# Performance work log

Measured on AMD Instinct MI355X. Metric: run time of the kernel, lower is better.

## Reference

```python
import jax, jax.numpy as jnp
import numpy as np

N_NODES = 100000
N_EDGES = 1600000
IN_F = 128
HID = 128
OUT = 2


def setup_inputs() -> dict:
    key = jax.random.key(0)
    ks = jax.random.split(key, 12)
    s = lambda k, sh, f: jax.random.normal(k, sh, dtype=jnp.float32) * (1.0 / np.sqrt(f))
    return {
        "x": jax.random.normal(ks[0], (N_NODES, IN_F), dtype=jnp.float32),
        "W_self1": s(ks[1], (IN_F, HID), IN_F),
        "W_neigh1": s(ks[2], (IN_F, HID), IN_F),
        "b1": jnp.zeros((HID,), dtype=jnp.float32),
        "W_self2": s(ks[3], (HID, HID), HID),
        "W_neigh2": s(ks[4], (HID, HID), HID),
        "b2": jnp.zeros((HID,), dtype=jnp.float32),
        "W_final": s(ks[5], (HID, OUT), HID),
        "b_final": jnp.zeros((OUT,), dtype=jnp.float32),
        "src": jax.random.randint(ks[6], (N_EDGES,), 0, N_NODES, dtype=jnp.int32),
        "dst": jax.random.randint(ks[7], (N_EDGES,), 0, N_NODES, dtype=jnp.int32),
    }


def _sage_mean(x, src, dst, n_nodes, W_self, W_neigh, b):
    # gather neighbor (src) features, scatter-mean onto dst nodes
    msg_sum = jax.ops.segment_sum(x[src], dst, num_segments=n_nodes)  # [N, F]
    deg = jax.ops.segment_sum(jnp.ones((src.shape[0],), x.dtype), dst,
                              num_segments=n_nodes)  # [N]
    h_neigh = msg_sum / jnp.maximum(deg, 1.0)[:, None]
    # DGL SAGEConv(mean): fc_self(h_self) + fc_neigh(h_neigh) (+ bias)
    return x @ W_self + h_neigh @ W_neigh + b


def reference(x, W_self1, W_neigh1, b1, W_self2, W_neigh2, b2,
              W_final, b_final, src, dst):
    n = x.shape[0]
    h = jax.nn.relu(_sage_mean(x, src, dst, n, W_self1, W_neigh1, b1))
    h = jax.nn.relu(_sage_mean(h, src, dst, n, W_self2, W_neigh2, b2))
    return h @ W_final + b_final  # [N, 2]
```

## Files before the change

kernel.cpp:

```cpp
#include <hip/hip_runtime.h>

#define N_NODES 100000
#define N_EDGES 1600000
#define F 128

#define BSHIFT 11
#define BNODES 2048
#define NBUCK 49
#define P1_BLOCKS 128
#define P1_TPB 256
#define EPB1 (N_EDGES / P1_BLOCKS)
#define CAPB 384
#define P2_TPB 1024

typedef _Float16 f16x8 __attribute__((ext_vector_type(8)));
typedef _Float16 f16x4 __attribute__((ext_vector_type(4)));
typedef float f32x4 __attribute__((ext_vector_type(4)));

__global__ __launch_bounds__(P1_TPB) void k_part(const int* __restrict__ src,
                                                 const int* __restrict__ dst,
                                                 int2* __restrict__ stage,
                                                 int* __restrict__ pcnt) {
    __shared__ int cnt[NBUCK];
    int t = threadIdx.x, blk = blockIdx.x;
    if (t < NBUCK) cnt[t] = 0;
    __syncthreads();
    int base = blk * EPB1;
    for (int i = t; i < EPB1; i += P1_TPB) {
        int e = base + i;
        int s = src[e], d = dst[e];
        int b = d >> BSHIFT;
        int pos = atomicAdd(&cnt[b], 1);
        if (pos < CAPB) stage[((long)b * P1_BLOCKS + blk) * CAPB + pos] = make_int2(s, d);
    }
    __syncthreads();
    if (t < NBUCK) pcnt[t * P1_BLOCKS + blk] = min(cnt[t], CAPB);
}

__global__ void k_bucketsum(const int* __restrict__ pcnt, int* __restrict__ bbase,
                            int* __restrict__ row_start) {
    __shared__ int tot[64];
    int b = threadIdx.x;
    int s = 0;
    if (b < NBUCK)
        for (int i = 0; i < P1_BLOCKS; i++) s += pcnt[b * P1_BLOCKS + i];
    tot[b] = s;
    __syncthreads();
    if (b == 0) {
        int acc = 0;
        for (int i = 0; i < NBUCK; i++) {
            bbase[i] = acc;
            acc += tot[i];
        }
        bbase[NBUCK] = acc;
        row_start[N_NODES] = acc;
    }
}

__global__ __launch_bounds__(P2_TPB) void k_build(const int2* __restrict__ stage,
                                                  const int* __restrict__ pcnt,
                                                  const int* __restrict__ bbase,
                                                  int* __restrict__ row_start,
                                                  int* __restrict__ esrc) {
    __shared__ int cnt[BNODES];
    __shared__ int scanw[P2_TPB / 64];
    int b = blockIdx.x, t = threadIdx.x;
    int nodeBase = b << BSHIFT;
    for (int i = t; i < BNODES; i += P2_TPB) cnt[i] = 0;
    __syncthreads();
    int grp = t >> 8, gt = t & 255;
    for (int s = grp; s < P1_BLOCKS; s += 4) {
        int n = pcnt[b * P1_BLOCKS + s];
        const int2* seg = &stage[((long)b * P1_BLOCKS + s) * CAPB];
        for (int i = gt; i < n; i += 256) atomicAdd(&cnt[seg[i].y & (BNODES - 1)], 1);
    }
    __syncthreads();
    int c0 = cnt[2 * t], c1 = cnt[2 * t + 1];
    int v = c0 + c1;
    int lane = t & 63, wv = t >> 6;
    int x = v;
#pragma unroll
    for (int off = 1; off < 64; off <<= 1) {
        int y = __shfl_up(x, off, 64);
        if (lane >= off) x += y;
    }
    if (lane == 63) scanw[wv] = x;
    __syncthreads();
    if (t == 0) {
        int acc = 0;
        for (int i = 0; i < P2_TPB / 64; i++) {
            int y = scanw[i];
            scanw[i] = acc;
            acc += y;
        }
    }
    __syncthreads();
    int excl = x - v + scanw[wv];
    int base0 = bbase[b];
    int n0 = nodeBase + 2 * t;
    if (n0 < N_NODES) row_start[n0] = base0 + excl;
    if (n0 + 1 < N_NODES) row_start[n0 + 1] = base0 + excl + c0;
    cnt[2 * t] = excl;
    cnt[2 * t + 1] = excl + c0;
    __syncthreads();
    for (int s = grp; s < P1_BLOCKS; s += 4) {
        int n = pcnt[b * P1_BLOCKS + s];
        const int2* seg = &stage[((long)b * P1_BLOCKS + s) * CAPB];
        for (int i = gt; i < n; i += 256) {
            int2 p = seg[i];
            int pos = atomicAdd(&cnt[p.y & (BNODES - 1)], 1);
            esrc[base0 + pos] = p.x;
        }
    }
}

__global__ void k_cast(const float* __restrict__ x, _Float16* __restrict__ xh, int n4) {
    int i = blockIdx.x * blockDim.x + threadIdx.x;
    if (i < n4) {
        float4 v = ((const float4*)x)[i];
        f16x4 h;
        h.x = (_Float16)v.x; h.y = (_Float16)v.y;
        h.z = (_Float16)v.z; h.w = (_Float16)v.w;
        ((f16x4*)xh)[i] = h;
    }
}

__global__ void k_prepw(const float* __restrict__ Ws, const float* __restrict__ Wn,
                        _Float16* __restrict__ Wt) {
    int i = blockIdx.x * blockDim.x + threadIdx.x;
    int n = i >> 8;
    int k = i & 255;
    float v = (k < 128) ? Ws[k * F + n] : Wn[(k - 128) * F + n];
    Wt[n * 256 + k] = (_Float16)v;
}

__global__ __launch_bounds__(256) void k_agg(const f16x4* __restrict__ xf,
                                             const int* __restrict__ row_start,
                                             const int* __restrict__ esrc,
                                             f16x4* __restrict__ out) {
    int wave = (int)((blockIdx.x * blockDim.x + threadIdx.x) >> 6);
    int lane = threadIdx.x & 63;
    if (wave >= N_NODES) return;
    int sub = lane >> 5, col = lane & 31;
    int beg = row_start[wave], end = row_start[wave + 1];
    float ax = 0.f, ay = 0.f, az = 0.f, aw = 0.f;
    int j = beg;
    for (; j + 4 <= end; j += 4) {
        int e0 = esrc[j + sub], e1 = esrc[j + 2 + sub];
        f16x4 v0 = xf[(long)e0 * 32 + col];
        f16x4 v1 = xf[(long)e1 * 32 + col];
        ax += (float)v0.x + (float)v1.x;
        ay += (float)v0.y + (float)v1.y;
        az += (float)v0.z + (float)v1.z;
        aw += (float)v0.w + (float)v1.w;
    }
    for (; j < end; j += 2) {
        if (j + sub < end) {
            f16x4 v = xf[(long)esrc[j + sub] * 32 + col];
            ax += (float)v.x; ay += (float)v.y; az += (float)v.z; aw += (float)v.w;
        }
    }
    ax += __shfl_xor(ax, 32, 64);
    ay += __shfl_xor(ay, 32, 64);
    az += __shfl_xor(az, 32, 64);
    aw += __shfl_xor(aw, 32, 64);
    if (sub == 0) {
        float inv = (end > beg) ? 1.0f / (float)(end - beg) : 0.0f;
        f16x4 r;
        r.x = (_Float16)(ax * inv);
        r.y = (_Float16)(ay * inv);
        r.z = (_Float16)(az * inv);
        r.w = (_Float16)(aw * inv);
        out[(long)wave * 32 + col] = r;
    }
}

template <bool FINAL>
__global__ __launch_bounds__(256, 2) void k_gemm_mfma(
    const _Float16* __restrict__ Aself, const _Float16* __restrict__ Aneigh,
    const _Float16* __restrict__ Wt, const float* __restrict__ bias,
    _Float16* __restrict__ Hout, const float* __restrict__ Wf,
    const float* __restrict__ bf, float* __restrict__ Out) {
    const int M = N_NODES;
    __shared__ _Float16 Wl[4096 * 8];
    int w = threadIdx.x >> 6;
    int lane = threadIdx.x & 63;
    int q = lane >> 4;
    int ln = lane & 15;
    int rBase = blockIdx.x * 128 + w * 32;

#pragma unroll
    for (int i = 0; i < 16; i++) {
        int s = threadIdx.x + i * 256;
        int L = s & 63, ct = (s >> 6) & 7, ks = s >> 9;
        int g = (ct * 16 + (L & 15)) * 256 + ks * 32 + (L >> 4) * 8;
        *(f16x8*)&Wl[s * 8] = *(const f16x8*)&Wt[g];
    }

    f32x4 acc[2][8];
#pragma unroll
    for (int rt = 0; rt < 2; rt++)
#pragma unroll
        for (int ct = 0; ct < 8; ct++) acc[rt][ct] = (f32x4){0.f, 0.f, 0.f, 0.f};

    __syncthreads();

    for (int ks = 0; ks < 8; ks++) {
        const _Float16* Abase = (ks < 4) ? Aself : Aneigh;
        int k0 = (ks & 3) * 32;
        f16x8 b[8];
#pragma unroll
        for (int ct = 0; ct < 8; ct++)
            b[ct] = *(const f16x8*)&Wl[((ks * 8 + ct) * 64 + lane) * 8];
#pragma unroll
        for (int rt = 0; rt < 2; rt++) {
            int row = rBase + rt * 16 + ln;
            f16x8 a = {};
            if (row < M) a = *(const f16x8*)&Abase[(long)row * F + k0 + q * 8];
#pragma unroll
            for (int ct = 0; ct < 8; ct++)
                acc[rt][ct] = __builtin_amdgcn_mfma_f32_16x16x32_f16(a, b[ct], acc[rt][ct], 0, 0, 0);
        }
    }

    float bv[8];
#pragma unroll
    for (int ct = 0; ct < 8; ct++) bv[ct] = bias[ct * 16 + ln];

    if (!FINAL) {
#pragma unroll
        for (int rt = 0; rt < 2; rt++) {
#pragma unroll
            for (int r = 0; r < 4; r++) {
                int row = rBase + rt * 16 + q * 4 + r;
                if (row < M) {
#pragma unroll
                    for (int ct = 0; ct < 8; ct++) {
                        float h = acc[rt][ct][r] + bv[ct];
                        h = h > 0.f ? h : 0.f;
                        Hout[(long)row * F + ct * 16 + ln] = (_Float16)h;
                    }
                }
            }
        }
    } else {
        float wf0[8], wf1[8];
#pragma unroll
        for (int ct = 0; ct < 8; ct++) {
            int c = ct * 16 + ln;
            wf0[ct] = Wf[c * 2 + 0];
            wf1[ct] = Wf[c * 2 + 1];
        }
        float bf0 = bf[0], bf1 = bf[1];
#pragma unroll
        for (int rt = 0; rt < 2; rt++) {
#pragma unroll
            for (int r = 0; r < 4; r++) {
                int row = rBase + rt * 16 + q * 4 + r;
                float p0 = 0.f, p1 = 0.f;
#pragma unroll
                for (int ct = 0; ct < 8; ct++) {
                    float h = acc[rt][ct][r] + bv[ct];
                    h = h > 0.f ? h : 0.f;
                    p0 += h * wf0[ct];
                    p1 += h * wf1[ct];
                }
#pragma unroll
                for (int off = 1; off < 16; off <<= 1) {
                    p0 += __shfl_xor(p0, off, 64);
                    p1 += __shfl_xor(p1, off, 64);
                }
                if (ln == 0 && row < M) {
                    Out[(long)row * 2 + 0] = p0 + bf0;
                    Out[(long)row * 2 + 1] = p1 + bf1;
                }
            }
        }
    }
}

extern "C" void kernel_launch(void* const* d_in, const int* in_sizes, int n_in,
                              void* d_out, int out_size, void* d_ws, size_t ws_size,
                              hipStream_t stream) {
    const float* x   = (const float*)d_in[0];
    const float* Ws1 = (const float*)d_in[1];
    const float* Wn1 = (const float*)d_in[2];
    const float* b1  = (const float*)d_in[3];
    const float* Ws2 = (const float*)d_in[4];
    const float* Wn2 = (const float*)d_in[5];
    const float* b2  = (const float*)d_in[6];
    const float* Wf  = (const float*)d_in[7];
    const float* bf  = (const float*)d_in[8];
    const int* src   = (const int*)d_in[9];
    const int* dst   = (const int*)d_in[10];
    float* out = (float*)d_out;

    char* ws = (char*)d_ws;
    int*      row_start = (int*)(ws + 0);
    int*      bbase     = (int*)(ws + 400016);
    int*      pcnt      = (int*)(ws + 400272);
    int2*     stage     = (int2*)(ws + 425360);
    int*      esrc      = (int*)(ws + 19692944);
    _Float16* xh        = (_Float16*)(ws + 26092944);
    _Float16* hneigh    = (_Float16*)(ws + 51692944);
    _Float16* h1        = (_Float16*)(ws + 77292944);
    _Float16* Wt1       = (_Float16*)(ws + 102892944);
    _Float16* Wt2       = (_Float16*)(ws + 102958480);

    const int TPB = 256;
    k_part<<<P1_BLOCKS, P1_TPB, 0, stream>>>(src, dst, stage, pcnt);
    k_bucketsum<<<1, 64, 0, stream>>>(pcnt, bbase, row_start);
    k_build<<<NBUCK, P2_TPB, 0, stream>>>(stage, pcnt, bbase, row_start, esrc);

    k_cast<<<(N_NODES * F / 4 + TPB - 1) / TPB, TPB, 0, stream>>>(x, xh, N_NODES * F / 4);
    k_prepw<<<128, 256, 0, stream>>>(Ws1, Wn1, Wt1);
    k_prepw<<<128, 256, 0, stream>>>(Ws2, Wn2, Wt2);

    k_agg<<<(N_NODES + 3) / 4, 256, 0, stream>>>((const f16x4*)xh, row_start, esrc,
                                                 (f16x4*)hneigh);
    k_gemm_mfma<false><<<(N_NODES + 127) / 128, 256, 0, stream>>>(
        xh, hneigh, Wt1, b1, h1, nullptr, nullptr, nullptr);
    k_agg<<<(N_NODES + 3) / 4, 256, 0, stream>>>((const f16x4*)h1, row_start, esrc,
                                                 (f16x4*)hneigh);
    k_gemm_mfma<true><<<(N_NODES + 127) / 128, 256, 0, stream>>>(
        h1, hneigh, Wt2, b2, nullptr, Wf, bf, out);
}
```

Measured before the change: 443.5 us.

## Store features in column-chunked planes so aggregation gathers stay cache-local

Feature matrices are now stored as 8 planes of 16 halves per node (chunk-major), and the cast, GEMM load/store and aggregation kernels are rewritten to use this layout. Aggregation is launched per chunk, so each block gathers from one 3.2 MB plane that can stay resident in cache. Each node is handled by 8 lanes, with lanes looping to the max degree in the wave. The two weight-prep launches are merged into one. The trade-off is that each gathered access is only 4 bytes, so memory transactions are smaller and more numerous, edge indices are re-read for every chunk, and divergent degrees leave lanes idle.

```diff
diff --git a/kernel.cpp b/kernel.cpp
--- a/kernel.cpp
+++ b/kernel.cpp
@@ -15,6 +15,7 @@
 
 typedef _Float16 f16x8 __attribute__((ext_vector_type(8)));
 typedef _Float16 f16x4 __attribute__((ext_vector_type(4)));
+typedef _Float16 f16x2 __attribute__((ext_vector_type(2)));
 typedef float f32x4 __attribute__((ext_vector_type(4)));
 
 __global__ __launch_bounds__(P1_TPB) void k_part(const int* __restrict__ src,
@@ -114,65 +115,64 @@
     }
 }
 
-__global__ void k_cast(const float* __restrict__ x, _Float16* __restrict__ xh, int n4) {
+__global__ void k_cast(const float* __restrict__ x, _Float16* __restrict__ xc) {
     int i = blockIdx.x * blockDim.x + threadIdx.x;
-    if (i < n4) {
-        float4 v = ((const float4*)x)[i];
-        f16x4 h;
-        h.x = (_Float16)v.x; h.y = (_Float16)v.y;
-        h.z = (_Float16)v.z; h.w = (_Float16)v.w;
-        ((f16x4*)xh)[i] = h;
-    }
-}
-
-__global__ void k_prepw(const float* __restrict__ Ws, const float* __restrict__ Wn,
-                        _Float16* __restrict__ Wt) {
+    int node = i >> 3, c = i & 7;
+    const float* xp = &x[(long)node * F + c * 16];
+    _Float16 h[16];
+#pragma unroll
+    for (int j = 0; j < 16; j++) h[j] = (_Float16)xp[j];
+    _Float16* op = &xc[((long)c * N_NODES + node) * 16];
+    *(f16x8*)op = *(f16x8*)&h[0];
+    *(f16x8*)(op + 8) = *(f16x8*)&h[8];
+}
+
+__global__ void k_prepw(const float* __restrict__ Ws1, const float* __restrict__ Wn1,
+                        const float* __restrict__ Ws2, const float* __restrict__ Wn2,
+                        _Float16* __restrict__ Wt1, _Float16* __restrict__ Wt2) {
     int i = blockIdx.x * blockDim.x + threadIdx.x;
-    int n = i >> 8;
-    int k = i & 255;
+    int which = i >> 15;
+    int j = i & 32767;
+    int n = j >> 8;
+    int k = j & 255;
+    const float* Ws = which ? Ws2 : Ws1;
+    const float* Wn = which ? Wn2 : Wn1;
+    _Float16* Wt = which ? Wt2 : Wt1;
     float v = (k < 128) ? Ws[k * F + n] : Wn[(k - 128) * F + n];
     Wt[n * 256 + k] = (_Float16)v;
 }
 
-__global__ __launch_bounds__(256) void k_agg(const f16x4* __restrict__ xf,
+__global__ __launch_bounds__(256) void k_agg(const _Float16* __restrict__ xc,
                                              const int* __restrict__ row_start,
                                              const int* __restrict__ esrc,
-                                             f16x4* __restrict__ out) {
-    int wave = (int)((blockIdx.x * blockDim.x + threadIdx.x) >> 6);
-    int lane = threadIdx.x & 63;
-    if (wave >= N_NODES) return;
-    int sub = lane >> 5, col = lane & 31;
-    int beg = row_start[wave], end = row_start[wave + 1];
-    float ax = 0.f, ay = 0.f, az = 0.f, aw = 0.f;
-    int j = beg;
-    for (; j + 4 <= end; j += 4) {
-        int e0 = esrc[j + sub], e1 = esrc[j + 2 + sub];
-        f16x4 v0 = xf[(long)e0 * 32 + col];
-        f16x4 v1 = xf[(long)e1 * 32 + col];
-        ax += (float)v0.x + (float)v1.x;
-        ay += (float)v0.y + (float)v1.y;
-        az += (float)v0.z + (float)v1.z;
-        aw += (float)v0.w + (float)v1.w;
-    }
-    for (; j < end; j += 2) {
-        if (j + sub < end) {
-            f16x4 v = xf[(long)esrc[j + sub] * 32 + col];
-            ax += (float)v.x; ay += (float)v.y; az += (float)v.z; aw += (float)v.w;
-        }
-    }
-    ax += __shfl_xor(ax, 32, 64);
-    ay += __shfl_xor(ay, 32, 64);
-    az += __shfl_xor(az, 32, 64);
-    aw += __shfl_xor(aw, 32, 64);
-    if (sub == 0) {
-        float inv = (end > beg) ? 1.0f / (float)(end - beg) : 0.0f;
-        f16x4 r;
-        r.x = (_Float16)(ax * inv);
-        r.y = (_Float16)(ay * inv);
-        r.z = (_Float16)(az * inv);
-        r.w = (_Float16)(aw * inv);
-        out[(long)wave * 32 + col] = r;
-    }
+                                             _Float16* __restrict__ outc) {
+    int c = blockIdx.x & 7;
+    int nb = blockIdx.x >> 3;
+    int w = threadIdx.x >> 6, lane = threadIdx.x & 63;
+    int nodesub = lane >> 3, colhalf = lane & 7;
+    int node = nb * 32 + w * 8 + nodesub;
+    int beg = row_start[node], end = row_start[node + 1];
+    int deg = end - beg;
+    int md = deg;
+    md = max(md, __shfl_xor(md, 8, 64));
+    md = max(md, __shfl_xor(md, 16, 64));
+    md = max(md, __shfl_xor(md, 32, 64));
+    const _Float16* plane = xc + (long)c * N_NODES * 16;
+    float ax = 0.f, ay = 0.f;
+    for (int i = 0; i < md; i++) {
+        int j = beg + i;
+        if (j < end) {
+            int s = esrc[j];
+            f16x2 v = *(const f16x2*)&plane[(long)s * 16 + colhalf * 2];
+            ax += (float)v.x;
+            ay += (float)v.y;
+        }
+    }
+    float inv = (deg > 0) ? 1.0f / (float)deg : 0.0f;
+    f16x2 r;
+    r.x = (_Float16)(ax * inv);
+    r.y = (_Float16)(ay * inv);
+    *(f16x2*)&outc[((long)c * N_NODES + node) * 16 + colhalf * 2] = r;
 }
 
 template <bool FINAL>
@@ -207,7 +207,9 @@
 
     for (int ks = 0; ks < 8; ks++) {
         const _Float16* Abase = (ks < 4) ? Aself : Aneigh;
-        int k0 = (ks & 3) * 32;
+        int kk = (ks & 3) * 32 + q * 8;
+        int chk = kk >> 4;
+        int inner = kk & 15;
         f16x8 b[8];
 #pragma unroll
         for (int ct = 0; ct < 8; ct++)
@@ -216,7 +218,7 @@
         for (int rt = 0; rt < 2; rt++) {
             int row = rBase + rt * 16 + ln;
             f16x8 a = {};
-            if (row < M) a = *(const f16x8*)&Abase[(long)row * F + k0 + q * 8];
+            if (row < M) a = *(const f16x8*)&Abase[((long)chk * N_NODES + row) * 16 + inner];
 #pragma unroll
             for (int ct = 0; ct < 8; ct++)
                 acc[rt][ct] = __builtin_amdgcn_mfma_f32_16x16x32_f16(a, b[ct], acc[rt][ct], 0, 0, 0);
@@ -238,7 +240,7 @@
                     for (int ct = 0; ct < 8; ct++) {
                         float h = acc[rt][ct][r] + bv[ct];
                         h = h > 0.f ? h : 0.f;
-                        Hout[(long)row * F + ct * 16 + ln] = (_Float16)h;
+                        Hout[((long)ct * N_NODES + row) * 16 + ln] = (_Float16)h;
                     }
                 }
             }
@@ -307,21 +309,17 @@
     _Float16* Wt1       = (_Float16*)(ws + 102892944);
     _Float16* Wt2       = (_Float16*)(ws + 102958480);
 
-    const int TPB = 256;
     k_part<<<P1_BLOCKS, P1_TPB, 0, stream>>>(src, dst, stage, pcnt);
     k_bucketsum<<<1, 64, 0, stream>>>(pcnt, bbase, row_start);
     k_build<<<NBUCK, P2_TPB, 0, stream>>>(stage, pcnt, bbase, row_start, esrc);
 
-    k_cast<<<(N_NODES * F / 4 + TPB - 1) / TPB, TPB, 0, stream>>>(x, xh, N_NODES * F / 4);
-    k_prepw<<<128, 256, 0, stream>>>(Ws1, Wn1, Wt1);
-    k_prepw<<<128, 256, 0, stream>>>(Ws2, Wn2, Wt2);
-
-    k_agg<<<(N_NODES + 3) / 4, 256, 0, stream>>>((const f16x4*)xh, row_start, esrc,
-                                                 (f16x4*)hneigh);
+    k_cast<<<3125, 256, 0, stream>>>(x, xh);
+    k_prepw<<<256, 256, 0, stream>>>(Ws1, Wn1, Ws2, Wn2, Wt1, Wt2);
+
+    k_agg<<<25000, 256, 0, stream>>>(xh, row_start, esrc, hneigh);
     k_gemm_mfma<false><<<(N_NODES + 127) / 128, 256, 0, stream>>>(
         xh, hneigh, Wt1, b1, h1, nullptr, nullptr, nullptr);
-    k_agg<<<(N_NODES + 3) / 4, 256, 0, stream>>>((const f16x4*)h1, row_start, esrc,
-                                                 (f16x4*)hneigh);
+    k_agg<<<25000, 256, 0, stream>>>(h1, row_start, esrc, hneigh);
     k_gemm_mfma<true><<<(N_NODES + 127) / 128, 256, 0, stream>>>(
         h1, hneigh, Wt2, b2, nullptr, Wf, bf, out);
 }
```

Result: slower. 550.9 us (+24.2%).
